# Kernel tuning notes

Measured on AMD Instinct MI355X. Metric: run time of the kernel, lower is better.

The kernel has to match this reference:

```python
import math
import jax, jax.numpy as jnp
import numpy as np

B, T, E, H = 4, 2048, 1024, 16
S = E // H
SCALE = 1.0 / math.sqrt(S)
LN_EPS = 1e-5


def setup_inputs() -> dict:
    key = jax.random.key(0)
    ks = jax.random.split(key, 5)
    w_std = 1.0 / math.sqrt(E)
    return {
        "x": jax.random.normal(ks[0], (B, T, E), jnp.float32),
        "Wq": jax.random.normal(ks[1], (E, E), jnp.float32) * w_std,
        "Wk": jax.random.normal(ks[2], (E, E), jnp.float32) * w_std,
        "Wv": jax.random.normal(ks[3], (E, E), jnp.float32) * w_std,
        "Wu": jax.random.normal(ks[4], (E, E), jnp.float32) * w_std,
        "bu": jnp.zeros((E,), jnp.float32),
        "q_gamma": jnp.ones((S,), jnp.float32),
        "q_beta": jnp.zeros((S,), jnp.float32),
        "k_gamma": jnp.ones((S,), jnp.float32),
        "k_beta": jnp.zeros((S,), jnp.float32),
    }


def _layernorm(x, gamma, beta):
    # normalize over last (head) dim, eps matches torch LayerNorm default
    mu = jnp.mean(x, axis=-1, keepdims=True)
    var = jnp.mean(jnp.square(x - mu), axis=-1, keepdims=True)
    return (x - mu) * jax.lax.rsqrt(var + LN_EPS) * gamma + beta


def reference(x, Wq, Wk, Wv, Wu, bu, q_gamma, q_beta, k_gamma, k_beta):
    b, t, e = x.shape
    h, s = H, S
    # torch Linear: y = x @ W^T ; split into heads [b, t, h, s]
    q = (x @ Wq.T).reshape(b, t, h, s)
    k = (x @ Wk.T).reshape(b, t, h, s)
    v = (x @ Wv.T).reshape(b, t, h, s)
    # kqnorm: LayerNorm over head dim s
    q = _layernorm(q, q_gamma, q_beta)
    k = _layernorm(k, k_gamma, k_beta)
    # scaled dot-product scores [b, h, t, t]
    dots = jnp.einsum("bthd,bThd->bhtT", q, k) * SCALE
    causal = jnp.tril(jnp.ones((t, t), dtype=bool))
    dots = jnp.where(causal, dots, jnp.finfo(dots.dtype).min)
    attn = jax.nn.softmax(dots, axis=-1)
    out = jnp.einsum("bhtT,bThd->bthd", attn, v).reshape(b, t, e)
    return out @ Wu.T + bu
```

## Files before the change

### kernel.cpp

```cpp
#include <hip/hip_runtime.h>
#include <hip/hip_bf16.h>
#include <stdint.h>
#include <stddef.h>


using bf16 = __hip_bfloat16;
typedef __attribute__((ext_vector_type(8))) short s16x8;
typedef __attribute__((ext_vector_type(4))) short s16x4;
typedef __attribute__((ext_vector_type(4))) float f32x4;

#define MFMA16(a, b, c) __builtin_amdgcn_mfma_f32_16x16x32_bf16((a), (b), (c), 0, 0, 0)

static __device__ __forceinline__ s16x8 ld8(const bf16* p) {
    return *reinterpret_cast<const s16x8*>(p);
}
static __device__ __forceinline__ s16x8 ld8s(const short* p) {
    return *reinterpret_cast<const s16x8*>(p);
}
static __device__ __forceinline__ s16x8 cvt8(const float* p) {
    f32x4 u = *reinterpret_cast<const f32x4*>(p);
    f32x4 v = *reinterpret_cast<const f32x4*>(p + 4);
    s16x8 r;
#pragma unroll
    for (int e = 0; e < 4; e++) {
        r[e]     = __builtin_bit_cast(short, __float2bfloat16(u[e]));
        r[e + 4] = __builtin_bit_cast(short, __float2bfloat16(v[e]));
    }
    return r;
}

static __device__ __forceinline__ void async16(short* lds, const bf16* g) {
    __builtin_amdgcn_global_load_lds(
        (const __attribute__((address_space(1))) unsigned int*)g,
        (__attribute__((address_space(3))) unsigned int*)lds, 16, 0, 0);
}

#define EE 1024

__global__ __launch_bounds__(256) void cvt_all(
    const float* __restrict__ w0, const float* __restrict__ w1,
    const float* __restrict__ w2, const float* __restrict__ w3,
    const float* __restrict__ x,
    bf16* __restrict__ o0, bf16* __restrict__ o1,
    bf16* __restrict__ o2, bf16* __restrict__ o3, bf16* __restrict__ xb)
{
    const int z = blockIdx.z;
    const float* s;
    bf16* d;
    if (z < 4) {
        s = (z == 0) ? w0 : (z == 1) ? w1 : (z == 2) ? w2 : w3;
        d = (z == 0) ? o0 : (z == 1) ? o1 : (z == 2) ? o2 : o3;
    } else {
        s = x  + (size_t)(z - 4) * 1048576;
        d = xb + (size_t)(z - 4) * 1048576;
    }
    size_t i = ((size_t)blockIdx.x * 256 + threadIdx.x) * 8;
    *reinterpret_cast<s16x8*>(d + i) = cvt8(s + i);
}

template <int AF32>
__global__ __launch_bounds__(256) void gemm_qkv_t(
    const float* __restrict__ xf, const bf16* __restrict__ xb,
    const bf16* __restrict__ Wq, const bf16* __restrict__ Wk, const bf16* __restrict__ Wv,
    bf16* __restrict__ Qb, bf16* __restrict__ Kb, bf16* __restrict__ Vb,
    const float* __restrict__ qg, const float* __restrict__ qbt,
    const float* __restrict__ kg, const float* __restrict__ kbt)
{
    const int z = blockIdx.z;
    const bf16* Bt = (z == 0) ? Wq : (z == 1) ? Wk : Wv;
    bf16* out      = (z == 0) ? Qb : (z == 1) ? Kb : Vb;
    const float* gamma = (z == 0) ? qg : kg;
    const float* beta  = (z == 0) ? qbt : kbt;
    const bool  ln     = (z < 2);
    const float oscale = (z == 0) ? 0.125f : 1.0f;

    constexpr int LASZ = AF32 ? 128 * 40 : 2 * 4096;
    __shared__ __align__(16) short lA[LASZ];
    __shared__ __align__(16) short lB[2 * 4096];

    const int tid  = threadIdx.x;
    const int lane = tid & 63;
    const int w    = tid >> 6;
    const int wr = w >> 1, wc = w & 1;
    const int lr = lane & 15, quad = lane >> 4;

    const int mi = blockIdx.x * 8 + (blockIdx.y & 7);
    const int ni = blockIdx.y >> 3;
    const int m0 = mi * 128;
    const int n0 = ni * 128;

    const int strow = w * 32 + (lane >> 2);
    const int stcol = (lane & 3) * 8;
    const bf16* bgl = Bt + (size_t)(n0 + strow) * EE + stcol;

    f32x4 acc[4][4];
#pragma unroll
    for (int i = 0; i < 4; i++)
#pragma unroll
        for (int j = 0; j < 4; j++) acc[i][j] = (f32x4){0.f, 0.f, 0.f, 0.f};

    if constexpr (AF32) {
        constexpr int SA = 40;
        const int sr  = tid >> 1;
        const int sc0 = (tid & 1) << 4;
        const float* ap = xf + (size_t)(m0 + sr) * EE + sc0;
        short* lap = lA + sr * SA + sc0;
        short* bl = lB + (w * 2) * 512;
        const short* lArd = lA + (wr * 64 + lr) * SA + quad * 8;
        const short* lBrd = lB + (wc * 64 + lr) * 32 + quad * 8;
        const bf16* bg = bgl;

        for (int kt = 0; kt < EE / 32; ++kt) {
            s16x8 a0 = cvt8(ap), a1 = cvt8(ap + 8);
            __syncthreads();
            *reinterpret_cast<s16x8*>(lap)     = a0;
            *reinterpret_cast<s16x8*>(lap + 8) = a1;
            async16(bl, bg);
            async16(bl + 512, bg + 16 * EE);
            ap += 32;
            bg += 32;
            __syncthreads();

            s16x8 af[4], bfr[4];
#pragma unroll
            for (int i = 0; i < 4; i++) af[i]  = ld8s(lArd + i * 16 * SA);
#pragma unroll
            for (int j = 0; j < 4; j++) bfr[j] = ld8s(lBrd + j * 16 * 32);
#pragma unroll
            for (int i = 0; i < 4; i++)
#pragma unroll
                for (int j = 0; j < 4; j++) acc[i][j] = MFMA16(af[i], bfr[j], acc[i][j]);
        }
    } else {
        const bf16* agl = xb + (size_t)(m0 + strow) * EE + stcol;
        short* const al0 = lA + w * 1024;
        short* const bl0 = lB + w * 1024;

#define QSTAGE(c, kt)                                                     \
    {                                                                     \
        short* al = al0 + (c) * 4096;                                     \
        short* bl = bl0 + (c) * 4096;                                     \
        const bf16* ag = agl + (kt) * 32;                                 \
        const bf16* bg = bgl + (kt) * 32;                                 \
        async16(al, ag); async16(al + 512, ag + 16 * EE);                 \
        async16(bl, bg); async16(bl + 512, bg + 16 * EE);                 \
    }

        QSTAGE(0, 0)
#pragma unroll 1
        for (int kt = 0; kt < EE / 32; ++kt) {
            const int c = kt & 1;
            if (kt < EE / 32 - 1) {
                QSTAGE(c ^ 1, kt + 1)
                asm volatile("s_waitcnt vmcnt(4)" ::: "memory");
            } else {
                asm volatile("s_waitcnt vmcnt(0)" ::: "memory");
            }
            __builtin_amdgcn_s_barrier();

            const short* lArd = lA + c * 4096 + (wr * 64 + lr) * 32 + quad * 8;
            const short* lBrd = lB + c * 4096 + (wc * 64 + lr) * 32 + quad * 8;
            s16x8 af[4], bfr[4];
#pragma unroll
            for (int i = 0; i < 4; i++) af[i]  = ld8s(lArd + i * 512);
#pragma unroll
            for (int j = 0; j < 4; j++) bfr[j] = ld8s(lBrd + j * 512);
            __builtin_amdgcn_sched_barrier(0);
            asm volatile("s_waitcnt lgkmcnt(0)" ::: "memory");
            __builtin_amdgcn_sched_barrier(0);
#pragma unroll
            for (int i = 0; i < 4; i++)
#pragma unroll
                for (int j = 0; j < 4; j++) acc[i][j] = MFMA16(af[i], bfr[j], acc[i][j]);
            __builtin_amdgcn_s_barrier();
        }
#undef QSTAGE
    }

    if (ln) {
        float g[4], bt[4];
#pragma unroll
        for (int j = 0; j < 4; j++) {
            g[j]  = gamma[j * 16 + lr];
            bt[j] = beta[j * 16 + lr];
        }
#pragma unroll
        for (int i = 0; i < 4; i++) {
#pragma unroll
            for (int r = 0; r < 4; r++) {
                float s1 = 0.f, s2 = 0.f;
#pragma unroll
                for (int j = 0; j < 4; j++) {
                    float v = acc[i][j][r];
                    s1 += v;
                    s2 += v * v;
                }
#pragma unroll
                for (int off = 1; off < 16; off <<= 1) {
                    s1 += __shfl_xor(s1, off);
                    s2 += __shfl_xor(s2, off);
                }
                float mu  = s1 * (1.f / 64.f);
                float var = s2 * (1.f / 64.f) - mu * mu;
                float rs  = rsqrtf(var + 1e-5f);
                int row = m0 + wr * 64 + i * 16 + quad * 4 + r;
#pragma unroll
                for (int j = 0; j < 4; j++) {
                    float v = ((acc[i][j][r] - mu) * rs * g[j] + bt[j]) * oscale;
                    out[(size_t)row * EE + n0 + wc * 64 + j * 16 + lr] = __float2bfloat16(v);
                }
            }
        }
    } else {
#pragma unroll
        for (int i = 0; i < 4; i++)
#pragma unroll
            for (int r = 0; r < 4; r++) {
                int row = m0 + wr * 64 + i * 16 + quad * 4 + r;
#pragma unroll
                for (int j = 0; j < 4; j++)
                    out[(size_t)row * EE + n0 + wc * 64 + j * 16 + lr] =
                        __float2bfloat16(acc[i][j][r]);
            }
    }
}

__global__ __launch_bounds__(512, 4) void flash(
    const bf16* __restrict__ Qb, const bf16* __restrict__ Kb,
    const bf16* __restrict__ Vb, bf16* __restrict__ Ob)
{
    const int flat = blockIdx.y * 8 + blockIdx.x;
    const int vid  = (flat & 7) * 64 + (flat >> 3);
    const int pr = vid & 7;
    const int bh = vid >> 3;
    const int b = bh >> 4, h = bh & 15;
    const int tid = threadIdx.x, lane = tid & 63, w = tid >> 6;
    const int lr = lane & 15, quad = lane >> 4;
    const size_t base = (size_t)b * 2048 * 1024 + h * 64;
    const float C  = 1.44269504088896340736f;
    const float M0 = 12.0f;

    __shared__ __align__(16) short VT[64 * 72];
    __shared__ __align__(16) short PT[128 * 72];
    __shared__ __align__(16) short KS[2][64 * 64];

    short* const prow = PT + (w * 16 + lr) * 72;
    const bf16* const kst = Kb + base + (size_t)(w * 8 + (lane >> 3)) * 1024 +
                            (((lane & 7) ^ (lane >> 3)) << 3);
    short* const kdst = &KS[0][0] + w * 512;
    const int kaddr0 = lr * 64 + ((quad ^ (lr & 7)) << 3);

#pragma unroll 1
    for (int ph = 0; ph < 2; ++ph) {
        const int qt = ph ? (15 - pr) : pr;
        const int tw = qt * 128 + w * 16;

        s16x8 qf[2];
#pragma unroll
        for (int ks = 0; ks < 2; ks++)
            qf[ks] = ld8(Qb + base + (size_t)(tw + lr) * 1024 + ks * 32 + quad * 8);

        f32x4 o[4];
#pragma unroll
        for (int j = 0; j < 4; j++) o[j] = (f32x4){0.f, 0.f, 0.f, 0.f};
        float lsum = 0.f;

        const int nkt = 2 * qt + 2;

        __syncthreads();
        s16x8 va0 = ld8(Vb + base + (size_t)lane * 1024 + w * 8);
        s16x8 vb0;
        async16(kdst, kst);

#define FTILE(KT, V0C, KCUR, V0N, KNXT)                                          \
    {                                                                            \
        const int kb = (KT) * 64;                                                \
        const bool active = (kb <= tw + 15);                                     \
        __syncthreads();   \
        _Pragma("unroll")                                                        \
        for (int e = 0; e < 8; e++)                                              \
            VT[(w * 8 + e) * 72 + lane] = V0C[e];                                \
        const int kb2 = kb + 64;                                                 \
        if (kb2 < nkt * 64) {        \
            async16(kdst + (KNXT) * 4096, kst + (size_t)kb2 * 1024);             \
            V0N = ld8(Vb + base + (size_t)(kb2 + lane) * 1024 + w * 8);          \
        }                                                                        \
        if (active) {                                                            \
            const short* kc = &KS[KCUR][0];                                      \
            f32x4 sc[4];                                                         \
            _Pragma("unroll")                                                    \
            for (int jk = 0; jk < 4; jk++) sc[jk] = (f32x4){0.f, 0.f, 0.f, 0.f}; \
            _Pragma("unroll")                                                    \
            for (int ks = 0; ks < 2; ks++)                                       \
                _Pragma("unroll")                                                \
                for (int jk = 0; jk < 4; jk++) {                                 \
                    s16x8 kf = ld8s(kc + jk * 1024 + (kaddr0 ^ (ks * 32)));      \
                    sc[jk] = MFMA16(kf, qf[ks], sc[jk]);                         \
                }                                                                \
            const bool needmask = (kb + 63 > tw);                                \
            const int qq = tw + lr;                                              \
            _Pragma("unroll")                                                    \
            for (int jk = 0; jk < 4; jk++) {                                     \
                s16x4 pk;                                                        \
                _Pragma("unroll")                                                \
                for (int r = 0; r < 4; r++) {                                    \
                    float p = exp2f(fmaf(sc[jk][r], C, -M0));                    \
                    if (needmask && (kb + jk * 16 + quad * 4 + r > qq))          \
                        p = 0.f;                                                 \
                    lsum += p;                                                   \
                    pk[r] = __builtin_bit_cast(short, __float2bfloat16(p));      \
                }                                                                \
                *reinterpret_cast<s16x4*>(prow + jk * 16 + quad * 4) = pk;       \
            }                                                                    \
        }                                                                        \
        __syncthreads();                                      \
        if (active) {                                                            \
            _Pragma("unroll")                                                    \
            for (int ks = 0; ks < 2; ks++) {                                     \
                s16x8 pf = ld8s(prow + ks * 32 + quad * 8);                      \
                s16x8 vf[4];                                                     \
                _Pragma("unroll")                                                \
                for (int j = 0; j < 4; j++)                                      \
                    vf[j] = ld8s(VT + (j * 16 + lr) * 72 + ks * 32 + quad * 8);  \
                _Pragma("unroll")                                                \
                for (int j = 0; j < 4; j++)                                      \
                    o[j] = MFMA16(pf, vf[j], o[j]);                              \
            }                                                                    \
        }                                                                        \
    }

#pragma unroll 1
        for (int kt = 0; kt < nkt; kt += 2) {
            FTILE(kt,     va0, 0, vb0, 1)
            FTILE(kt + 1, vb0, 1, va0, 0)
        }
#undef FTILE

        float l = lsum;
        l += __shfl_xor(l, 16);
        l += __shfl_xor(l, 32);
#pragma unroll
        for (int r = 0; r < 4; r++) {
            float inv = 1.f / __shfl(l, quad * 4 + r);
            int t = tw + quad * 4 + r;
#pragma unroll
            for (int j = 0; j < 4; j++)
                Ob[base + (size_t)t * 1024 + j * 16 + lr] =
                    __float2bfloat16(o[j][r] * inv);
        }
    }
}

__global__ __launch_bounds__(256) void gemm_bias(
    const bf16* __restrict__ A, const bf16* __restrict__ Bt,
    const float* __restrict__ bias, float* __restrict__ out)
{
    __shared__ __align__(16) short lA[2 * 4096];
    __shared__ __align__(16) short lB[2 * 4096];

    const int tid  = threadIdx.x;
    const int lane = tid & 63;
    const int w    = tid >> 6;
    const int wr = w >> 1, wc = w & 1;
    const int lr = lane & 15, quad = lane >> 4;

    const int mi = blockIdx.x * 8 + (blockIdx.y & 7);
    const int ni = blockIdx.y >> 3;
    const int m0 = mi * 128;
    const int n0 = ni * 128;

    const int strow = w * 32 + (lane >> 2);
    const int stcol = (lane & 3) * 8;
    const bf16* agl = A  + (size_t)(m0 + strow) * EE + stcol;
    const bf16* bgl = Bt + (size_t)(n0 + strow) * EE + stcol;
    short* const al0 = lA + w * 1024;
    short* const bl0 = lB + w * 1024;

    f32x4 acc[4][4];
#pragma unroll
    for (int i = 0; i < 4; i++)
#pragma unroll
        for (int j = 0; j < 4; j++) acc[i][j] = (f32x4){0.f, 0.f, 0.f, 0.f};

#define BSTAGE(c, kt)                                                     \
    {                                                                     \
        short* al = al0 + (c) * 4096;                                     \
        short* bl = bl0 + (c) * 4096;                                     \
        const bf16* ag = agl + (kt) * 32;                                 \
        const bf16* bg = bgl + (kt) * 32;                                 \
        async16(al, ag); async16(al + 512, ag + 16 * EE);                 \
        async16(bl, bg); async16(bl + 512, bg + 16 * EE);                 \
    }

    BSTAGE(0, 0)
#pragma unroll 1
    for (int kt = 0; kt < EE / 32; ++kt) {
        const int c = kt & 1;
        if (kt < EE / 32 - 1) {
            BSTAGE(c ^ 1, kt + 1)
            asm volatile("s_waitcnt vmcnt(4)" ::: "memory");
        } else {
            asm volatile("s_waitcnt vmcnt(0)" ::: "memory");
        }
        __builtin_amdgcn_s_barrier();

        const short* lArd = lA + c * 4096 + (wr * 64 + lr) * 32 + quad * 8;
        const short* lBrd = lB + c * 4096 + (wc * 64 + lr) * 32 + quad * 8;
        s16x8 af[4], bfr[4];
#pragma unroll
        for (int i = 0; i < 4; i++) af[i]  = ld8s(lArd + i * 512);
#pragma unroll
        for (int j = 0; j < 4; j++) bfr[j] = ld8s(lBrd + j * 512);
        __builtin_amdgcn_sched_barrier(0);
        asm volatile("s_waitcnt lgkmcnt(0)" ::: "memory");
        __builtin_amdgcn_sched_barrier(0);
#pragma unroll
        for (int i = 0; i < 4; i++)
#pragma unroll
            for (int j = 0; j < 4; j++) acc[i][j] = MFMA16(af[i], bfr[j], acc[i][j]);
        __builtin_amdgcn_s_barrier();
    }
#undef BSTAGE

    float bz[4];
#pragma unroll
    for (int j = 0; j < 4; j++)
        bz[j] = bias[n0 + wc * 64 + j * 16 + lr];
#pragma unroll
    for (int i = 0; i < 4; i++)
#pragma unroll
        for (int r = 0; r < 4; r++) {
            int row = m0 + wr * 64 + i * 16 + quad * 4 + r;
#pragma unroll
            for (int j = 0; j < 4; j++)
                out[(size_t)row * EE + n0 + wc * 64 + j * 16 + lr] =
                    acc[i][j][r] + bz[j];
        }
}

extern "C" void kernel_launch(void* const* d_in, const int* in_sizes, int n_in,
                              void* d_out, int out_size, void* d_ws, size_t ws_size,
                              hipStream_t stream)
{
    (void)in_sizes; (void)n_in; (void)out_size;
    const float* x   = (const float*)d_in[0];
    const float* Wq  = (const float*)d_in[1];
    const float* Wk  = (const float*)d_in[2];
    const float* Wv  = (const float*)d_in[3];
    const float* Wu  = (const float*)d_in[4];
    const float* bu  = (const float*)d_in[5];
    const float* qg  = (const float*)d_in[6];
    const float* qbt = (const float*)d_in[7];
    const float* kg  = (const float*)d_in[8];
    const float* kbt = (const float*)d_in[9];
    float* out = (float*)d_out;

    bf16* Qb  = (bf16*)d_ws;
    bf16* Kb  = Qb  + (size_t)8192 * 1024;
    bf16* Vb  = Kb  + (size_t)8192 * 1024;
    bf16* Wqb = Vb  + (size_t)8192 * 1024;
    bf16* Wkb = Wqb + (size_t)1024 * 1024;
    bf16* Wvb = Wkb + (size_t)1024 * 1024;
    bf16* Wub = Wvb + (size_t)1024 * 1024;
    bf16* xb  = Wub + (size_t)1024 * 1024;

    const size_t need = ((size_t)3 * 8192 * 1024 + 4 * 1024 * 1024 + 8192 * 1024) * 2;
    const bool fast = ws_size >= need;

    cvt_all<<<dim3(512, 1, fast ? 12 : 4), 256, 0, stream>>>(
        Wq, Wk, Wv, Wu, x, Wqb, Wkb, Wvb, Wub, xb);
    if (fast)
        gemm_qkv_t<0><<<dim3(8, 64, 3), 256, 0, stream>>>(
            x, xb, Wqb, Wkb, Wvb, Qb, Kb, Vb, qg, qbt, kg, kbt);
    else
        gemm_qkv_t<1><<<dim3(8, 64, 3), 256, 0, stream>>>(
            x, nullptr, Wqb, Wkb, Wvb, Qb, Kb, Vb, qg, qbt, kg, kbt);
    flash<<<dim3(8, 64), 512, 0, stream>>>(Qb, Kb, Vb, Qb);
    gemm_bias<<<dim3(8, 64), 256, 0, stream>>>(Qb, Wub, bu, out);
}
```

Before: 284.0 us.

## Split barriers into explicit waitcnt plus s_barrier, add setprio and packed bf16 convert

Each __syncthreads in the flash-attention tile loop becomes an explicit s_waitcnt on the one counter that matters (vmcnt, then lgkmcnt) followed by a raw s_barrier. MFMA blocks are wrapped in s_setprio to raise wave priority. The softmax exp loop is split into masked and unmasked branches and uses the v_cvt_pk_bf16_f32 packed convert. The aim is less barrier and conversion overhead and better MFMA issue. The first barrier waits only on vmcnt, so correctness depends on the prior LDS ordering and the async global_load_lds being covered by that wait.

```diff
diff --git a/kernel.cpp b/kernel.cpp
--- a/kernel.cpp
+++ b/kernel.cpp
@@ -26,6 +26,11 @@
         r[e]     = __builtin_bit_cast(short, __float2bfloat16(u[e]));
         r[e + 4] = __builtin_bit_cast(short, __float2bfloat16(v[e]));
     }
+    return r;
+}
+static __device__ __forceinline__ unsigned int cvtpk(float lo, float hi) {
+    unsigned int r;
+    asm("v_cvt_pk_bf16_f32 %0, %1, %2" : "=v"(r) : "v"(lo), "v"(hi));
     return r;
 }
 
@@ -276,12 +281,13 @@
     {                                                                            \
         const int kb = (KT) * 64;                                                \
         const bool active = (kb <= tw + 15);                                     \
-        __syncthreads();   \
+        asm volatile("s_waitcnt vmcnt(0)" ::: "memory");      \
+        __builtin_amdgcn_s_barrier();       \
         _Pragma("unroll")                                                        \
         for (int e = 0; e < 8; e++)                                              \
             VT[(w * 8 + e) * 72 + lane] = V0C[e];                                \
         const int kb2 = kb + 64;                                                 \
-        if (kb2 < nkt * 64) {        \
+        if (kb2 < nkt * 64) {       \
             async16(kdst + (KNXT) * 4096, kst + (size_t)kb2 * 1024);             \
             V0N = ld8(Vb + base + (size_t)(kb2 + lane) * 1024 + w * 8);          \
         }                                                                        \
@@ -290,6 +296,7 @@
             f32x4 sc[4];                                                         \
             _Pragma("unroll")                                                    \
             for (int jk = 0; jk < 4; jk++) sc[jk] = (f32x4){0.f, 0.f, 0.f, 0.f}; \
+            __builtin_amdgcn_s_setprio(1);                                       \
             _Pragma("unroll")                                                    \
             for (int ks = 0; ks < 2; ks++)                                       \
                 _Pragma("unroll")                                                \
@@ -297,23 +304,39 @@
                     s16x8 kf = ld8s(kc + jk * 1024 + (kaddr0 ^ (ks * 32)));      \
                     sc[jk] = MFMA16(kf, qf[ks], sc[jk]);                         \
                 }                                                                \
-            const bool needmask = (kb + 63 > tw);                                \
-            const int qq = tw + lr;                                              \
-            _Pragma("unroll")                                                    \
-            for (int jk = 0; jk < 4; jk++) {                                     \
-                s16x4 pk;                                                        \
+            __builtin_amdgcn_s_setprio(0);                                       \
+            if (kb + 63 > tw) {                  \
+                const int qq = tw + lr;                                          \
                 _Pragma("unroll")                                                \
-                for (int r = 0; r < 4; r++) {                                    \
-                    float p = exp2f(fmaf(sc[jk][r], C, -M0));                    \
-                    if (needmask && (kb + jk * 16 + quad * 4 + r > qq))          \
-                        p = 0.f;                                                 \
-                    lsum += p;                                                   \
-                    pk[r] = __builtin_bit_cast(short, __float2bfloat16(p));      \
+                for (int jk = 0; jk < 4; jk++) {                                 \
+                    const int k0 = kb + jk * 16 + quad * 4;                      \
+                    float p0 = exp2f(fmaf(sc[jk][0], C, -M0));                   \
+                    float p1 = exp2f(fmaf(sc[jk][1], C, -M0));                   \
+                    float p2 = exp2f(fmaf(sc[jk][2], C, -M0));                   \
+                    float p3 = exp2f(fmaf(sc[jk][3], C, -M0));                   \
+                    if (k0 + 0 > qq) p0 = 0.f;                                   \
+                    if (k0 + 1 > qq) p1 = 0.f;                                   \
+                    if (k0 + 2 > qq) p2 = 0.f;                                   \
+                    if (k0 + 3 > qq) p3 = 0.f;                                   \
+                    lsum += (p0 + p1) + (p2 + p3);                               \
+                    uint2 pk = {cvtpk(p0, p1), cvtpk(p2, p3)};                   \
+                    *reinterpret_cast<uint2*>(prow + jk * 16 + quad * 4) = pk;   \
                 }                                                                \
-                *reinterpret_cast<s16x4*>(prow + jk * 16 + quad * 4) = pk;       \
+            } else {                                 \
+                _Pragma("unroll")                                                \
+                for (int jk = 0; jk < 4; jk++) {                                 \
+                    float p0 = exp2f(fmaf(sc[jk][0], C, -M0));                   \
+                    float p1 = exp2f(fmaf(sc[jk][1], C, -M0));                   \
+                    float p2 = exp2f(fmaf(sc[jk][2], C, -M0));                   \
+                    float p3 = exp2f(fmaf(sc[jk][3], C, -M0));                   \
+                    lsum += (p0 + p1) + (p2 + p3);                               \
+                    uint2 pk = {cvtpk(p0, p1), cvtpk(p2, p3)};                   \
+                    *reinterpret_cast<uint2*>(prow + jk * 16 + quad * 4) = pk;   \
+                }                                                                \
             }                                                                    \
         }                                                                        \
-        __syncthreads();                                      \
+        asm volatile("s_waitcnt lgkmcnt(0)" ::: "memory");    \
+        __builtin_amdgcn_s_barrier();                  \
         if (active) {                                                            \
             _Pragma("unroll")                                                    \
             for (int ks = 0; ks < 2; ks++) {                                     \
@@ -322,9 +345,11 @@
                 _Pragma("unroll")                                                \
                 for (int j = 0; j < 4; j++)                                      \
                     vf[j] = ld8s(VT + (j * 16 + lr) * 72 + ks * 32 + quad * 8);  \
+                __builtin_amdgcn_s_setprio(1);                                   \
                 _Pragma("unroll")                                                \
                 for (int j = 0; j < 4; j++)                                      \
                     o[j] = MFMA16(pf, vf[j], o[j]);                              \
+                __builtin_amdgcn_s_setprio(0);                                   \
             }                                                                    \
         }                                                                        \
     }
```

Result: faster. 278.1 us (-2.1%).
